# Kernel optimization log

Hardware: AMD Instinct MI355X
Metric: run time of the kernel (lower is better)

The kernel has to match this reference:

```python
import jax, jax.numpy as jnp
import numpy as np

B, N, H, KRATE = 128, 400, 128, 0.2
EPS = 1e-9


def setup_inputs() -> dict:
    key = jax.random.key(0)
    ks = jax.random.split(key, 16)
    # correlation-like input: symmetric, values in (-1,1), unit diagonal
    x = jax.random.normal(ks[0], (B, N, N), dtype=jnp.float32)
    x = jnp.tanh(0.3 * x)
    x = 0.5 * (x + x.transpose(0, 2, 1))
    eye = jnp.eye(N, dtype=jnp.float32)
    x = x * (1.0 - eye) + eye

    def lin(k, fan_in, shape):
        return jax.random.normal(k, shape, dtype=jnp.float32) / np.sqrt(fan_in).astype(np.float32)

    return {
        "x": x,
        "slength": jnp.full((B,), 100, dtype=jnp.int32),
        # AE denoiser (num_of_node=N, hidden=H)
        "enc1_w": lin(ks[1], N, (N, H)), "enc1_b": jnp.zeros((H,), jnp.float32),
        "enc2_w": lin(ks[2], N, (N, H)), "enc2_b": jnp.zeros((H,), jnp.float32),
        "dec2_w": lin(ks[3], H, (H, N)), "dec2_b": jnp.zeros((N,), jnp.float32),
        "dec1_w": lin(ks[4], H, (H, N)), "dec1_b": jnp.zeros((N,), jnp.float32),
        # GCN predictor
        "gcn1_w": lin(ks[5], N, (N, H)), "gcn1_b": jnp.zeros((H,), jnp.float32),
        "gcn2_w": lin(ks[6], H, (H, H)), "gcn2_b": jnp.zeros((H,), jnp.float32),
        # classification head Linear(128 -> 2)
        "fc_w": lin(ks[7], H, (H, 2)), "fc_b": jnp.zeros((2,), jnp.float32),
    }


def reference(x, slength, enc1_w, enc1_b, enc2_w, enc2_b, dec2_w, dec2_b,
              dec1_w, dec1_b, gcn1_w, gcn1_b, gcn2_w, gcn2_b, fc_w, fc_b):
    eye = jnp.eye(N, dtype=x.dtype)

    # fisher transform + normalize by [0,0] entry
    xf = 0.5 * jnp.log((1.0 + x + EPS) / (1.0 - x + EPS))
    xf = xf / xf[:, 0, 0][:, None, None]

    # --- DA / AE denoiser: deltax = AE(xf), symmetrized ---
    out1 = jax.nn.relu(jnp.einsum('bij,jh->bih', xf, enc1_w) + enc1_b).transpose(0, 2, 1)  # [B,H,N]
    out2 = jax.nn.relu(jnp.einsum('bhn,nk->bhk', out1, enc2_w) + enc2_b)                   # [B,H,H]
    out2 = jax.nn.relu(jnp.einsum('bhk,kn->bhn', out2, dec2_w) + dec2_b + out1)            # [B,H,N]
    out2 = out2.transpose(0, 2, 1)                                                         # [B,N,H]
    delta = jnp.einsum('bnh,hm->bnm', out2, dec1_w) + dec1_b                               # [B,N,N]
    delta = 0.5 * (delta + delta.transpose(0, 2, 1))
    x2 = xf + delta * (1.0 - eye)

    # --- predictor on detached x2 ---
    xp = jax.lax.stop_gradient(x2)

    # topk sparsification at rate 0.2 over flattened NxN per sample
    k = int(N * N * KRATE)
    flat = xp.reshape(B, N * N)
    _, idx = jax.lax.top_k(flat, k)
    mask = jnp.zeros((B, N * N), xp.dtype).at[jnp.arange(B)[:, None], idx].set(1.0)
    A = xp * mask.reshape(B, N, N)

    # GCN norm (PyG gcn_norm with add_remaining_self_loops, fill=1)
    diag = jnp.diagonal(A, axis1=1, axis2=2)
    A = A + eye[None] * jnp.where(diag == 0.0, 1.0, 0.0)[:, :, None]
    deg = A.sum(axis=1)                      # scatter of edge weight on col index
    dinv = deg ** -0.5
    dinv = jnp.where(jnp.isinf(dinv), 0.0, dinv)
    An = dinv[:, :, None] * A * dinv[:, None, :]  # An[b,i,j] = dinv[i]*A[i,j]*dinv[j]

    # GCNConv1 -> ReLU -> GCNConv2 (aggregate onto col/target index)
    h = jax.nn.relu(jnp.einsum('bij,bif->bjf', An, xp @ gcn1_w) + gcn1_b)  # [B,N,H]
    h = jnp.einsum('bij,bif->bjf', An, h @ gcn2_w) + gcn2_b                # [B,N,H]

    pooled = h.mean(axis=1)                  # mean over nodes -> [B,H]
    out = jax.nn.relu(pooled) @ fc_w + fc_b  # [B,2]
    return out
```

## Files before the change

### kernel.cpp

```cpp
#include <hip/hip_runtime.h>
#include <hip/hip_bf16.h>
#include <math.h>

#define BATCH 128
#define NNODE 400
#define HID   128
#define NN    (NNODE*NNODE)
#define KSEL  32000
#define EQCAP 1024
#define EPSF  1e-9f
#define TSPLIT 8
#define SEG   (NN / TSPLIT)
#define NT    7
#define KC400 14
#define FRAGS (KC400*4096)
#define PLA   57344

__device__ __forceinline__ unsigned tokey(float f) {
  unsigned u = __float_as_uint(f);
  return (u & 0x80000000u) ? ~u : (u | 0x80000000u);
}

__device__ __forceinline__ short f2bf(float f) {
  unsigned u = __float_as_uint(f);
  u += 0x7fffu + ((u >> 16) & 1u);
  return (short)(u >> 16);
}
__device__ __forceinline__ float bf2f(short s) {
  return __uint_as_float(((unsigned)(unsigned short)s) << 16);
}

__device__ __forceinline__ float xfhw(float xv, float cmul) {
  float la = __builtin_amdgcn_logf(1.0f + xv + EPSF);
  float lb = __builtin_amdgcn_logf(1.0f - xv + EPSF);
  return (la - lb) * cmul;
}

typedef __attribute__((ext_vector_type(8))) short s8v;
typedef __attribute__((ext_vector_type(4))) short s4v;
typedef __attribute__((ext_vector_type(4))) float f4v;

#define BK 16
#define LP 68

template<bool AT, bool BIAS, bool RES, bool RELU, bool TS>
__global__ void __launch_bounds__(256) gemm64(
    const float* __restrict__ A, long sA, int lda,
    const float* __restrict__ B, long sB, int ldb,
    const float* __restrict__ bias,
    const float* __restrict__ Res, long sRes,
    float* __restrict__ C, long sC, int ldc,
    int M, int Nc, int K)
{
  __shared__ float As[BK][LP];
  __shared__ float Bs[BK][LP];
  const int bz = blockIdx.z;
  A += (size_t)bz * sA;
  B += (size_t)bz * sB;
  C += (size_t)bz * sC;
  const float* Rp = RES ? (Res + (size_t)bz * sRes) : nullptr;

  const int n0 = blockIdx.x * 64;
  const int m0 = blockIdx.y * 64;
  const int tid = threadIdx.x;
  const int tx = tid & 15, ty = tid >> 4;
  const bool edgeM = (m0 + 64 > M);
  const bool edgeN = (n0 + 64 > Nc);

  float acc[4][4];
#pragma unroll
  for (int i = 0; i < 4; ++i)
#pragma unroll
    for (int j = 0; j < 4; ++j) acc[i][j] = 0.f;

  for (int k0 = 0; k0 < K; k0 += BK) {
    if (!AT) {
      const int m = tid & 63, g = tid >> 6;
      if (!edgeM) {
        const float4 v = *(const float4*)(A + (size_t)(m0 + m) * lda + k0 + 4 * g);
        As[4 * g + 0][m] = v.x; As[4 * g + 1][m] = v.y;
        As[4 * g + 2][m] = v.z; As[4 * g + 3][m] = v.w;
      } else {
        const int gm = m0 + m;
        const bool ok = gm < M;
#pragma unroll
        for (int j = 0; j < 4; ++j)
          As[4 * g + j][m] = ok ? A[(size_t)gm * lda + k0 + 4 * g + j] : 0.f;
      }
    } else {
      const int k = tid >> 4, mg = tid & 15;
      if (!edgeM) {
        const float4 v = *(const float4*)(A + (size_t)(k0 + k) * lda + m0 + 4 * mg);
        *(float4*)&As[k][4 * mg] = v;
      } else {
#pragma unroll
        for (int j = 0; j < 4; ++j) {
          const int gm = m0 + 4 * mg + j;
          As[k][4 * mg + j] = (gm < M) ? A[(size_t)(k0 + k) * lda + gm] : 0.f;
        }
      }
    }
    {
      const int k = tid >> 4, ng = tid & 15;
      if (!edgeN) {
        const float4 v = *(const float4*)(B + (size_t)(k0 + k) * ldb + n0 + 4 * ng);
        *(float4*)&Bs[k][4 * ng] = v;
      } else {
#pragma unroll
        for (int j = 0; j < 4; ++j) {
          const int gn = n0 + 4 * ng + j;
          Bs[k][4 * ng + j] = (gn < Nc) ? B[(size_t)(k0 + k) * ldb + gn] : 0.f;
        }
      }
    }
    __syncthreads();
#pragma unroll
    for (int kk = 0; kk < BK; ++kk) {
      const float4 a = *(const float4*)&As[kk][ty << 2];
      const float4 b = *(const float4*)&Bs[kk][tx << 2];
      const float av[4] = {a.x, a.y, a.z, a.w};
      const float bv[4] = {b.x, b.y, b.z, b.w};
#pragma unroll
      for (int i = 0; i < 4; ++i)
#pragma unroll
        for (int j = 0; j < 4; ++j) acc[i][j] += av[i] * bv[j];
    }
    __syncthreads();
  }

#pragma unroll
  for (int i = 0; i < 4; ++i) {
    const int m = m0 + (ty << 2) + i;
    if (m >= M) continue;
#pragma unroll
    for (int j = 0; j < 4; ++j) {
      const int n = n0 + (tx << 2) + j;
      if (n >= Nc) continue;
      float v = acc[i][j];
      if (BIAS) v += bias[n];
      const size_t loc = TS ? ((size_t)n * ldc + m) : ((size_t)m * ldc + n);
      if (RES) v += Rp[loc];
      if (RELU) v = fmaxf(v, 0.f);
      C[loc] = v;
    }
  }
}

__global__ void bsplit5(
    const float* __restrict__ gcn1_w, const float* __restrict__ gcn2_w,
    const float* __restrict__ enc1_w, const float* __restrict__ enc2_w,
    const float* __restrict__ dec1_w,
    short* __restrict__ w1frag, short* __restrict__ w2frag,
    short* __restrict__ e1frag, short* __restrict__ e2frag,
    short* __restrict__ dfrag) {
  const float* W; short* out; int K, Kpad, N, Npad;
  switch (blockIdx.y) {
    case 0: W = gcn1_w; out = w1frag; K = NNODE; Kpad = 448; N = HID;   Npad = 128; break;
    case 1: W = gcn2_w; out = w2frag; K = HID;   Kpad = 128; N = HID;   Npad = 128; break;
    case 2: W = enc1_w; out = e1frag; K = NNODE; Kpad = 448; N = HID;   Npad = 128; break;
    case 3: W = enc2_w; out = e2frag; K = NNODE; Kpad = 448; N = HID;   Npad = 128; break;
    default: W = dec1_w; out = dfrag; K = HID;   Kpad = 128; N = NNODE; Npad = 448; break;
  }
  int t = blockIdx.x * 256 + threadIdx.x;
  if (t >= Kpad * Npad) return;
  int k = t / Npad, n = t - k * Npad;
  float v = (k < K && n < N) ? W[(size_t)k * N + n] : 0.f;
  short hi = f2bf(v);
  short lo = f2bf(v - bf2f(hi));
  int ntiles = Npad >> 4;
  size_t idx = (((size_t)(k >> 5) * ntiles + (n >> 4)) * 64
                + (((k >> 3) & 3) * 16 + (n & 15))) * 8 + (k & 7);
  size_t PL = (size_t)(Kpad >> 5) * ntiles * 512;
  out[idx] = hi;
  out[PL + idx] = lo;
}

template<bool AT, bool FRAG, bool BIAS, bool RELU, bool SCL, bool TS, bool XF>
__global__ void __launch_bounds__(256) mfgemm(
    const float* __restrict__ A, long sA, int lda,
    const short* __restrict__ Bf, long sB, int kc,
    const float* __restrict__ bias,
    const float* __restrict__ scl,
    float* __restrict__ Cf, long sCf, int ldc,
    short* __restrict__ Cfrag, long sCfrag, int okc,
    const float* __restrict__ denomp, float* __restrict__ xfout,
    int M, int K)
{
  __shared__ float As[64][68];
  const int bz = blockIdx.y;
  A += (size_t)bz * sA;
  Bf += (size_t)bz * sB;
  if (SCL) scl += (size_t)bz * NNODE;
  if (!FRAG) Cf += (size_t)bz * sCf;
  else       Cfrag += (size_t)bz * sCfrag;
  if (XF) xfout += (size_t)bz * sA;
  const float cmul = XF ? (0.34657359027997264f / denomp[bz]) : 0.f;

  const int tid = threadIdx.x;
  const int lane = tid & 63, wave = tid >> 6;
  const int wqm = wave >> 1, wqn = wave & 1;
  const int quad = lane >> 4, l15 = lane & 15;
  const int m0 = blockIdx.x * 64;

  f4v acc[2][4];
#pragma unroll
  for (int i = 0; i < 2; ++i)
#pragma unroll
    for (int j = 0; j < 4; ++j) acc[i][j] = (f4v){0.f, 0.f, 0.f, 0.f};

  const int nstage = (K + 63) >> 6;
  for (int st = 0; st < nstage; ++st) {
    const int k0 = st << 6;
    if (st) __syncthreads();
    if (!AT) {
      const int mrow = tid >> 4;
      const int k4 = (tid & 15) << 2;
#pragma unroll
      for (int u = 0; u < 4; ++u) {
        const int m = mrow + (u << 4);
        const int gm = m0 + m, gk = k0 + k4;
        float4 v = {0.f, 0.f, 0.f, 0.f};
        if (gm < M) {
          if (gk + 4 <= K) {
            float4 xv = *(const float4*)(A + (size_t)gm * lda + gk);
            if (XF) {
              v.x = xfhw(xv.x, cmul);
              v.y = xfhw(xv.y, cmul);
              v.z = xfhw(xv.z, cmul);
              v.w = xfhw(xv.w, cmul);
              *(float4*)(xfout + (size_t)gm * lda + gk) = v;
            } else v = xv;
          } else {
            float* pv = (float*)&v;
#pragma unroll
            for (int j = 0; j < 4; ++j)
              if (gk + j < K) {
                float xv = A[(size_t)gm * lda + gk + j];
                if (XF) {
                  pv[j] = xfhw(xv, cmul);
                  xfout[(size_t)gm * lda + gk + j] = pv[j];
                } else pv[j] = xv;
              }
          }
        }
        *(float4*)&As[m][k4] = v;
      }
    } else {
      const int kk = tid >> 4;
      const int m4 = (tid & 15) << 2;
#pragma unroll
      for (int u = 0; u < 4; ++u) {
        const int gk = k0 + kk + (u << 4);
        float4 v = {0.f, 0.f, 0.f, 0.f};
        if (gk < K) {
          if (m0 + m4 + 4 <= M) v = *(const float4*)(A + (size_t)gk * lda + m0 + m4);
          else {
            float* pv = (float*)&v;
#pragma unroll
            for (int j = 0; j < 4; ++j)
              if (m0 + m4 + j < M) pv[j] = A[(size_t)gk * lda + m0 + m4 + j];
          }
        }
        As[m4 + 0][kk + (u << 4)] = v.x;
        As[m4 + 1][kk + (u << 4)] = v.y;
        As[m4 + 2][kk + (u << 4)] = v.z;
        As[m4 + 3][kk + (u << 4)] = v.w;
      }
    }
    __syncthreads();

#pragma unroll
    for (int c2 = 0; c2 < 2; ++c2) {
      const int c = (st << 1) + c2;
      s8v bhi[4], blo[4];
#pragma unroll
      for (int nt = 0; nt < 4; ++nt) {
        const int ntg = (wqn << 2) + nt;
        const size_t off = (((size_t)c * 8 + ntg) * 64 + lane) * 8;
        bhi[nt] = *(const s8v*)(Bf + off);
        blo[nt] = *(const s8v*)(Bf + (size_t)kc * 4096 + off);
      }
#pragma unroll
      for (int mt = 0; mt < 2; ++mt) {
        const int row = (wqm << 5) + (mt << 4) + l15;
        const int kof = (c2 << 5) + (quad << 3);
        const f4v a0 = *(const f4v*)&As[row][kof];
        const f4v a1 = *(const f4v*)&As[row][kof + 4];
        s8v ah, al;
#pragma unroll
        for (int j = 0; j < 4; ++j) {
          short h0 = f2bf(a0[j]); ah[j] = h0; al[j] = f2bf(a0[j] - bf2f(h0));
          short h1 = f2bf(a1[j]); ah[j + 4] = h1; al[j + 4] = f2bf(a1[j] - bf2f(h1));
        }
#pragma unroll
        for (int nt = 0; nt < 4; ++nt) {
          acc[mt][nt] = __builtin_amdgcn_mfma_f32_16x16x32_bf16(ah, bhi[nt], acc[mt][nt], 0, 0, 0);
          acc[mt][nt] = __builtin_amdgcn_mfma_f32_16x16x32_bf16(ah, blo[nt], acc[mt][nt], 0, 0, 0);
          acc[mt][nt] = __builtin_amdgcn_mfma_f32_16x16x32_bf16(al, bhi[nt], acc[mt][nt], 0, 0, 0);
        }
      }
    }
  }

  if (TS) {
    for (int nh = 0; nh < 2; ++nh) {
      __syncthreads();
      if (wqn == nh) {
#pragma unroll
        for (int mt = 0; mt < 2; ++mt)
#pragma unroll
          for (int nt = 0; nt < 4; ++nt) {
            const int tn = (nt << 4) + l15;
            const int n  = (wqn << 6) + tn;
            const int mc = (wqm << 5) + (mt << 4) + (quad << 2);
            const f4v a = acc[mt][nt];
#pragma unroll
            for (int reg = 0; reg < 4; ++reg) {
              float v = a[reg];
              if (SCL) v *= scl[m0 + mc + reg];
              if (BIAS) v += bias[n];
              if (RELU) v = fmaxf(v, 0.f);
              As[tn][mc + reg] = v;
            }
          }
      }
      __syncthreads();
      const int row = tid >> 2, cq = tid & 3;
#pragma unroll
      for (int u = 0; u < 4; ++u) {
        const int col = (cq + (u << 2)) << 2;
        if (m0 + col + 4 <= M) {
          const float4 v = *(const float4*)&As[row][col];
          *(float4*)(Cf + (size_t)((nh << 6) + row) * ldc + m0 + col) = v;
        }
      }
    }
    return;
  }

#pragma unroll
  for (int mt = 0; mt < 2; ++mt) {
    const int mb = m0 + (wqm << 5) + (mt << 4) + (quad << 2);
#pragma unroll
    for (int nt = 0; nt < 4; ++nt) {
      const int n = (wqn << 6) + (nt << 4) + l15;
      const f4v a = acc[mt][nt];
      if (!FRAG) {
#pragma unroll
        for (int reg = 0; reg < 4; ++reg) {
          const int m = mb + reg;
          if (m < M) {
            float v = a[reg];
            if (SCL) v *= scl[m];
            if (BIAS) v += bias[n];
            if (RELU) v = fmaxf(v, 0.f);
            Cf[(size_t)m * ldc + n] = v;
          }
        }
      } else {
        s4v h4, l4;
#pragma unroll
        for (int reg = 0; reg < 4; ++reg) {
          const int m = mb + reg;
          float v = (m < M) ? (SCL ? a[reg] * scl[m] : a[reg]) : 0.f;
          short hh = f2bf(v);
          h4[reg] = hh; l4[reg] = f2bf(v - bf2f(hh));
        }
        const int chunkT = mb >> 5, quadT = (mb >> 3) & 3, jT0 = mb & 7;
        const size_t off = (((size_t)chunkT * 8 + (wqn << 2) + nt) * 64
                            + quadT * 16 + l15) * 8 + jT0;
        *(s4v*)(Cfrag + off) = h4;
        *(s4v*)(Cfrag + (size_t)okc * 4096 + off) = l4;
      }
    }
  }
}

__global__ void __launch_bounds__(256) g4mf(
    const float* __restrict__ o1,
    const short* __restrict__ wfrag,
    const float* __restrict__ bias,
    float* __restrict__ xf,
    unsigned* __restrict__ ghist)
{
  __shared__ float D2[64][68];
  __shared__ unsigned hist[2048];
  const int b = blockIdx.y;
  int p = blockIdx.x, bi = 0;
  while (p >= NT - bi) { p -= NT - bi; ++bi; }
  const int bj = bi + p;
  const int I0 = bi * 64, J0 = bj * 64;
  const bool diag = (bi == bj);

  o1 += (size_t)b * HID * NNODE;
  xf += (size_t)b * NN;
  unsigned* gh = ghist + (size_t)b * 4096;

  const int tid = threadIdx.x;
  const int lane = tid & 63, wave = tid >> 6;
  const int wq = wave & 1;
  const bool d1 = wave < 2;
  const int Bt = (d1 ? bj : bi) * 4;
  const int quad = lane >> 4, l15 = lane & 15;
  const int M0 = d1 ? I0 : J0;

  for (int i = tid; i < 2048; i += 256) hist[i] = 0u;

  f4v acc[2][4];
#pragma unroll
  for (int i = 0; i < 2; ++i)
#pragma unroll
    for (int j = 0; j < 4; ++j) acc[i][j] = (f4v){0.f, 0.f, 0.f, 0.f};

  const int gm0 = M0 + (wq << 5) + l15;

  for (int c = 0; c < 4; ++c) {
    const int k0 = c << 5;
    s8v bhi[4], blo[4];
#pragma unroll
    for (int nt = 0; nt < 4; ++nt) {
      const int ntg = Bt + nt;
      const size_t off = (((size_t)c * 28 + ntg) * 64 + lane) * 8;
      bhi[nt] = *(const s8v*)(wfrag + off);
      blo[nt] = *(const s8v*)(wfrag + PLA + off);
    }
#pragma unroll
    for (int mt = 0; mt < 2; ++mt) {
      const int gm = gm0 + (mt << 4);
      float av[8];
      if (gm < NNODE) {
        const float* cp = o1 + (size_t)(k0 + (quad << 3)) * NNODE + gm;
#pragma unroll
        for (int j = 0; j < 8; ++j) av[j] = cp[(size_t)j * NNODE];
      } else {
#pragma unroll
        for (int j = 0; j < 8; ++j) av[j] = 0.f;
      }
      s8v ah, al;
#pragma unroll
      for (int j = 0; j < 8; ++j) {
        short h = f2bf(av[j]); ah[j] = h; al[j] = f2bf(av[j] - bf2f(h));
      }
#pragma unroll
      for (int nt = 0; nt < 4; ++nt) {
        acc[mt][nt] = __builtin_amdgcn_mfma_f32_16x16x32_bf16(ah, bhi[nt], acc[mt][nt], 0, 0, 0);
        acc[mt][nt] = __builtin_amdgcn_mfma_f32_16x16x32_bf16(ah, blo[nt], acc[mt][nt], 0, 0, 0);
        acc[mt][nt] = __builtin_amdgcn_mfma_f32_16x16x32_bf16(al, bhi[nt], acc[mt][nt], 0, 0, 0);
      }
    }
  }

  if (!d1) {
#pragma unroll
    for (int mt = 0; mt < 2; ++mt) {
      const int mb = (wq << 5) + (mt << 4) + (quad << 2);
#pragma unroll
      for (int nt = 0; nt < 4; ++nt) {
        const int nn = (nt << 4) + l15;
        const f4v a = acc[mt][nt];
#pragma unroll
        for (int reg = 0; reg < 4; ++reg) D2[mb + reg][nn] = a[reg];
      }
    }
  }
  __syncthreads();

  if (d1) {
    const unsigned w = diag ? 1u : 2u;
#pragma unroll
    for (int mt = 0; mt < 2; ++mt) {
      const int a0 = (wq << 5) + (mt << 4) + (quad << 2);
#pragma unroll
      for (int nt = 0; nt < 4; ++nt) {
        const int nn = (nt << 4) + l15;
        const int gj = J0 + nn;
        const f4v d1v = acc[mt][nt];
        const f4v d2t = *(const f4v*)&D2[nn][a0];
        f4v vv;
#pragma unroll
        for (int reg = 0; reg < 4; ++reg) {
          const int gi = I0 + a0 + reg;
          float v = 0.f;
          if (gi < NNODE && gj < NNODE) {
            v = xf[(size_t)gi * NNODE + gj];
            if (gi != gj)
              v += 0.5f * (d1v[reg] + d2t[reg] + bias[gj] + bias[gi]);
            const unsigned bin = tokey(v) >> 20;
            atomicAdd(&hist[bin >> 1], w << ((bin & 1) << 4));
          }
          vv[reg] = v;
        }
#pragma unroll
        for (int reg = 0; reg < 4; ++reg) {
          const int gi = I0 + a0 + reg;
          if (gi < NNODE && gj < NNODE) xf[(size_t)gi * NNODE + gj] = vv[reg];
        }
        if (!diag && gj < NNODE && (I0 + a0 + 4 <= NNODE)) {
          *(float4*)(xf + (size_t)gj * NNODE + I0 + a0) = *(float4*)&vv;
        }
      }
    }
  }
  __syncthreads();
  for (int i = tid; i < 2048; i += 256) {
    const unsigned v = hist[i];
    const unsigned lo = v & 0xFFFFu, hi = v >> 16;
    if (lo) atomicAdd(&gh[2 * i], lo);
    if (hi) atomicAdd(&gh[2 * i + 1], hi);
  }
}

__global__ void tzd(const float* __restrict__ x, unsigned* __restrict__ ghist,
                    unsigned* __restrict__ sprefix, int* __restrict__ sk,
                    int* __restrict__ eqcnt, float* __restrict__ deg,
                    float* __restrict__ denom) {
  int t = blockIdx.x * 256 + threadIdx.x;
  if (t < BATCH * 4096) ghist[t] = 0u;
  if (t < BATCH) {
    sprefix[t] = 0u; sk[t] = KSEL; eqcnt[t] = 0;
    float v = x[(size_t)t * NN];
    denom[t] = 0.5f * logf((1.0f + v + EPSF) / (1.0f - v + EPSF));
  }
  if (t < BATCH * NNODE) deg[t] = 0.f;
}

__global__ void __launch_bounds__(256) thistA(const float* __restrict__ x2,
                                              const unsigned* __restrict__ sprefix,
                                              unsigned* __restrict__ ghist) {
  __shared__ unsigned h[4096];
  const int b  = blockIdx.y;
  const int sb = blockIdx.x;
  const int tid = threadIdx.x;
  for (int i = tid; i < 4096; i += 256) h[i] = 0u;
  __syncthreads();

  const unsigned prefix = sprefix[b];
  const float4* p4 = (const float4*)(x2 + (size_t)b * NN);
  const int i0 = sb * (SEG / 4), i1 = i0 + (SEG / 4);
  for (int i = i0 + tid; i < i1; i += 256) {
    float4 v = p4[i];
    unsigned k0 = tokey(v.x), k1 = tokey(v.y), k2 = tokey(v.z), k3 = tokey(v.w);
    if ((k0 & 0xFFF00000u) == prefix) atomicAdd(&h[(k0 >> 8) & 4095u], 1u);
    if ((k1 & 0xFFF00000u) == prefix) atomicAdd(&h[(k1 >> 8) & 4095u], 1u);
    if ((k2 & 0xFFF00000u) == prefix) atomicAdd(&h[(k2 >> 8) & 4095u], 1u);
    if ((k3 & 0xFFF00000u) == prefix) atomicAdd(&h[(k3 >> 8) & 4095u], 1u);
  }
  __syncthreads();
  for (int i = tid; i < 4096; i += 256) {
    unsigned s = h[i];
    if (s) atomicAdd(&ghist[(size_t)b * 4096 + i], s);
  }
}

__global__ void __launch_bounds__(256) thistB(const float* __restrict__ x2,
                                              const unsigned* __restrict__ sprefix,
                                              unsigned* __restrict__ ghist) {
  __shared__ unsigned h[8][256];
  const int b  = blockIdx.y;
  const int sb = blockIdx.x;
  const int tid = threadIdx.x;
  for (int i = tid; i < 8 * 256; i += 256) ((unsigned*)h)[i] = 0u;
  __syncthreads();

  const unsigned prefix = sprefix[b];
  const int rep = tid & 7;
  const float4* p4 = (const float4*)(x2 + (size_t)b * NN);
  const int i0 = sb * (SEG / 4), i1 = i0 + (SEG / 4);
  for (int i = i0 + tid; i < i1; i += 256) {
    float4 v = p4[i];
    unsigned k0 = tokey(v.x), k1 = tokey(v.y), k2 = tokey(v.z), k3 = tokey(v.w);
    if ((k0 & 0xFFFFFF00u) == prefix) atomicAdd(&h[rep][k0 & 255u], 1u);
    if ((k1 & 0xFFFFFF00u) == prefix) atomicAdd(&h[rep][k1 & 255u], 1u);
    if ((k2 & 0xFFFFFF00u) == prefix) atomicAdd(&h[rep][k2 & 255u], 1u);
    if ((k3 & 0xFFFFFF00u) == prefix) atomicAdd(&h[rep][k3 & 255u], 1u);
  }
  __syncthreads();
  if (tid < 256) {
    unsigned s = h[0][tid] + h[1][tid] + h[2][tid] + h[3][tid]
               + h[4][tid] + h[5][tid] + h[6][tid] + h[7][tid];
    if (s) atomicAdd(&ghist[(size_t)b * 4096 + tid], s);
  }
}

template<int SH>
__global__ void __launch_bounds__(256) tpick12(unsigned* __restrict__ ghist,
                                               unsigned* __restrict__ sprefix,
                                               int* __restrict__ sk) {
  const int b = blockIdx.x;
  __shared__ unsigned h[4096];
  __shared__ unsigned csum[256];
  unsigned* gh = ghist + (size_t)b * 4096;
  unsigned local = 0;
#pragma unroll
  for (int u = 0; u < 16; ++u) {
    unsigned v = gh[threadIdx.x * 16 + u];
    h[threadIdx.x * 16 + u] = v;
    local += v;
  }
  csum[threadIdx.x] = local;
  __syncthreads();
  if (threadIdx.x == 0) {
    int k = sk[b];
    int bin = 0;
    for (int ch = 255; ch >= 0; --ch) {
      int S = (int)csum[ch];
      if (S >= k) {
        for (int bb = ch * 16 + 15; bb >= ch * 16; --bb) {
          int c = (int)h[bb];
          if (c >= k) { bin = bb; break; }
          k -= c;
        }
        break;
      }
      k -= S;
    }
    sprefix[b] = sprefix[b] | ((unsigned)bin << SH);
    sk[b] = k;
  }
#pragma unroll
  for (int u = 0; u < 16; ++u) gh[threadIdx.x * 16 + u] = 0u;
}

__global__ void __launch_bounds__(256) tpick8f(const unsigned* __restrict__ ghist,
                                               const unsigned* __restrict__ sprefix,
                                               const int* __restrict__ sk,
                                               unsigned* __restrict__ tau,
                                               int* __restrict__ rrem) {
  const int b = blockIdx.x;
  __shared__ unsigned h[256];
  h[threadIdx.x] = ghist[(size_t)b * 4096 + threadIdx.x];
  __syncthreads();
  if (threadIdx.x == 0) {
    int k = sk[b];
    unsigned byte = 0u;
    for (int bin = 255; bin >= 0; --bin) {
      int c = (int)h[bin];
      if (c >= k) { byte = (unsigned)bin; break; }
      k -= c;
    }
    tau[b] = sprefix[b] | byte;
    rrem[b] = k;
  }
}

__global__ void __launch_bounds__(256) build_kc(
    const float* __restrict__ x2, const unsigned* __restrict__ tau,
    float* __restrict__ A, float* __restrict__ deg,
    int* __restrict__ eqcnt, int* __restrict__ eqidx) {
  __shared__ float cs[NNODE];
  const int b = blockIdx.y, rg = blockIdx.x;
  const int tid = threadIdx.x;
  for (int i = tid; i < NNODE; i += 256) cs[i] = 0.f;
  __syncthreads();
  const unsigned tk = tau[b];
  const size_t base = (size_t)b * NN + (size_t)rg * 6400;
  for (int u = 0; u < 25; ++u) {
    const int t = u * 256 + tid;
    const float v = x2[base + t];
    const unsigned key = tokey(v);
    const float a = (key > tk) ? v : 0.f;
    A[base + t] = a;
    if (key == tk) {
      int p = atomicAdd(&eqcnt[b], 1);
      if (p < EQCAP) eqidx[b * EQCAP + p] = rg * 6400 + t;
    }
    if (a != 0.f) atomicAdd(&cs[t % NNODE], a);
  }
  __syncthreads();
  for (int j = tid; j < NNODE; j += 256)
    if (cs[j] != 0.f) atomicAdd(&deg[b * NNODE + j], cs[j]);
}

__global__ void __launch_bounds__(256) eqdinv(
    float* __restrict__ A, const float* __restrict__ x2,
    float* __restrict__ deg, float* __restrict__ dinv,
    const int* __restrict__ eqcnt, const int* __restrict__ eqidx,
    const int* __restrict__ rrem) {
  const int b = blockIdx.x;
  int cnt = eqcnt[b]; if (cnt > EQCAP) cnt = EQCAP;
  const int r = rrem[b];
  for (int t = threadIdx.x; t < cnt; t += 256) {
    int idx = eqidx[b * EQCAP + t];
    int rank = 0;
    for (int u = 0; u < cnt; ++u) rank += (eqidx[b * EQCAP + u] < idx) ? 1 : 0;
    if (rank < r) {
      float v = x2[(size_t)b * NN + idx];
      A[(size_t)b * NN + idx] = v;
      atomicAdd(&deg[b * NNODE + idx % NNODE], v);
    }
  }
  __syncthreads();
  for (int j = threadIdx.x; j < NNODE; j += 256) {
    float d = deg[b * NNODE + j];
    size_t o = (size_t)b * NN + (size_t)j * NNODE + j;
    if (A[o] == 0.f) { A[o] = 1.0f; d += 1.0f; }
    dinv[b * NNODE + j] = (d == 0.f) ? 0.f : 1.0f / sqrtf(d);
  }
}

__global__ void head_k(const float* __restrict__ h2, const float* __restrict__ fc_w,
                       const float* __restrict__ fc_b, float* __restrict__ out) {
  int b = blockIdx.x;
  int f = threadIdx.x;
  float s = 0.f;
  const float* p = h2 + (size_t)b * NNODE * HID + f;
  for (int j = 0; j < NNODE; ++j) s += p[(size_t)j * HID];
  float pv = fmaxf(s / (float)NNODE, 0.f);
  __shared__ float r0[128], r1[128];
  r0[f] = pv * fc_w[f * 2 + 0];
  r1[f] = pv * fc_w[f * 2 + 1];
  __syncthreads();
  for (int sft = 64; sft > 0; sft >>= 1) {
    if (f < sft) { r0[f] += r0[f + sft]; r1[f] += r1[f + sft]; }
    __syncthreads();
  }
  if (f == 0) {
    out[b * 2 + 0] = r0[0] + fc_b[0];
    out[b * 2 + 1] = r1[0] + fc_b[1];
  }
}

extern "C" void kernel_launch(void* const* d_in, const int* in_sizes, int n_in,
                              void* d_out, int out_size, void* d_ws, size_t ws_size,
                              hipStream_t stream) {
  const float* x      = (const float*)d_in[0];
  const float* enc1_w = (const float*)d_in[2];
  const float* enc1_b = (const float*)d_in[3];
  const float* enc2_w = (const float*)d_in[4];
  const float* enc2_b = (const float*)d_in[5];
  const float* dec2_w = (const float*)d_in[6];
  const float* dec2_b = (const float*)d_in[7];
  const float* dec1_w = (const float*)d_in[8];
  const float* dec1_b = (const float*)d_in[9];
  const float* gcn1_w = (const float*)d_in[10];
  const float* gcn1_b = (const float*)d_in[11];
  const float* gcn2_w = (const float*)d_in[12];
  const float* gcn2_b = (const float*)d_in[13];
  const float* fc_w   = (const float*)d_in[14];
  const float* fc_b   = (const float*)d_in[15];
  float* out = (float*)d_out;
  (void)in_sizes; (void)n_in; (void)out_size; (void)ws_size;

  float* ws = (float*)d_ws;
  size_t off = 0;
  auto take = [&](size_t n) { float* p = ws + off; off += (n + 63) & ~(size_t)63; return p; };
  float* xf   = take((size_t)BATCH * NN);
  float* dl   = take((size_t)BATCH * NN);
  float* o1   = take((size_t)BATCH * HID * NNODE);
  float* o2   = take((size_t)BATCH * HID * HID);
  float* hbuf = take((size_t)BATCH * NNODE * HID);
  float* denom = take(BATCH);
  float* dinv  = take((size_t)BATCH * NNODE);
  float* deg   = take((size_t)BATCH * NNODE);
  unsigned* tau = (unsigned*)take(BATCH);
  int* rrem  = (int*)take(BATCH);
  int* eqcnt = (int*)take(BATCH);
  int* eqidx = (int*)take((size_t)BATCH * EQCAP);
  unsigned* ghist   = (unsigned*)take((size_t)BATCH * 4096);
  unsigned* sprefix = (unsigned*)take(BATCH);
  int*      sk      = (int*)take(BATCH);
  short* w1frag = (short*)take((size_t)FRAGS + 64);
  short* w2frag = (short*)take((size_t)4 * 4096 + 64);
  short* e1frag = (short*)take((size_t)FRAGS + 64);
  short* e2frag = (short*)take((size_t)FRAGS + 64);
  short* dfrag  = (short*)take((size_t)PLA + 64);
  short* xwfrag = (short*)o1;
  const long sXW = 2L * FRAGS;

  tzd<<<2048, 256, 0, stream>>>(x, ghist, sprefix, sk, eqcnt, deg, denom);
  bsplit5<<<dim3(224, 5), 256, 0, stream>>>(gcn1_w, gcn2_w, enc1_w, enc2_w, dec1_w,
                                            w1frag, w2frag, e1frag, e2frag, dfrag);

  mfgemm<false, false, true, true, false, true, true><<<dim3(7, BATCH), 256, 0, stream>>>(
      x, NN, NNODE, e1frag, 0, KC400, enc1_b, nullptr,
      o1, (long)HID * NNODE, NNODE, nullptr, 0, 0, denom, xf, NNODE, NNODE);
  mfgemm<false, false, true, true, false, false, false><<<dim3(2, BATCH), 256, 0, stream>>>(
      o1, (long)HID * NNODE, NNODE, e2frag, 0, KC400, enc2_b, nullptr,
      o2, (long)HID * HID, HID, nullptr, 0, 0, nullptr, nullptr, HID, NNODE);
  gemm64<false, true, true, true, false><<<dim3(7, 2, BATCH), 256, 0, stream>>>(
      o2, (long)HID * HID, HID, dec2_w, 0, NNODE, dec2_b,
      o1, (long)HID * NNODE, o1, (long)HID * NNODE, NNODE, HID, NNODE, HID);

  g4mf<<<dim3(NT * (NT + 1) / 2, BATCH), 256, 0, stream>>>(o1, dfrag, dec1_b, xf, ghist);

  tpick12<20><<<BATCH, 256, 0, stream>>>(ghist, sprefix, sk);
  thistA<<<dim3(TSPLIT, BATCH), 256, 0, stream>>>(xf, sprefix, ghist);
  tpick12<8><<<BATCH, 256, 0, stream>>>(ghist, sprefix, sk);
  thistB<<<dim3(TSPLIT, BATCH), 256, 0, stream>>>(xf, sprefix, ghist);
  tpick8f<<<BATCH, 256, 0, stream>>>(ghist, sprefix, sk, tau, rrem);

  build_kc<<<dim3(25, BATCH), 256, 0, stream>>>(xf, tau, dl, deg, eqcnt, eqidx);
  eqdinv<<<BATCH, 256, 0, stream>>>(dl, xf, deg, dinv, eqcnt, eqidx, rrem);

  mfgemm<false, true, false, false, true, false, false><<<dim3(7, BATCH), 256, 0, stream>>>(
      xf, NN, NNODE, w1frag, 0, KC400, nullptr, dinv,
      nullptr, 0, 128, xwfrag, sXW, KC400, nullptr, nullptr, NNODE, NNODE);
  mfgemm<true, false, true, true, true, false, false><<<dim3(7, BATCH), 256, 0, stream>>>(
      dl, NN, NNODE, xwfrag, sXW, KC400, gcn1_b, dinv,
      hbuf, (long)NNODE * HID, HID, nullptr, 0, 0, nullptr, nullptr, NNODE, NNODE);
  mfgemm<false, true, false, false, true, false, false><<<dim3(7, BATCH), 256, 0, stream>>>(
      hbuf, (long)NNODE * HID, HID, w2frag, 0, 4, nullptr, dinv,
      nullptr, 0, 128, xwfrag, sXW, KC400, nullptr, nullptr, NNODE, HID);
  mfgemm<true, false, true, false, true, false, false><<<dim3(7, BATCH), 256, 0, stream>>>(
      dl, NN, NNODE, xwfrag, sXW, KC400, gcn2_b, dinv,
      hbuf, (long)NNODE * HID, HID, nullptr, 0, 0, nullptr, nullptr, NNODE, NNODE);

  head_k<<<BATCH, HID, 0, stream>>>(hbuf, fc_w, fc_b, out);
}
```

Measured before the change: 651.6 us.

## Compact radix-select candidates in pass A to skip a full rescan in pass B

The second histogram pass now writes the keys that match the 12-bit prefix into a per-sample candidate buffer (reusing the dl workspace), using wave ballot and an atomic counter. The final 8-bit histogram and threshold pick are fused into one kernel that reads only those candidates instead of rescanning the full NxN matrix. This removes one full read of x2 per sample and one kernel launch. In exchange it adds global atomics and scattered writes in thistA, and the fused pick kernel runs one block per sample.

```diff
diff --git a/kernel.cpp b/kernel.cpp
--- a/kernel.cpp
+++ b/kernel.cpp
@@ -513,11 +513,11 @@
 __global__ void tzd(const float* __restrict__ x, unsigned* __restrict__ ghist,
                     unsigned* __restrict__ sprefix, int* __restrict__ sk,
                     int* __restrict__ eqcnt, float* __restrict__ deg,
-                    float* __restrict__ denom) {
+                    float* __restrict__ denom, unsigned* __restrict__ ccnt) {
   int t = blockIdx.x * 256 + threadIdx.x;
   if (t < BATCH * 4096) ghist[t] = 0u;
   if (t < BATCH) {
-    sprefix[t] = 0u; sk[t] = KSEL; eqcnt[t] = 0;
+    sprefix[t] = 0u; sk[t] = KSEL; eqcnt[t] = 0; ccnt[t] = 0u;
     float v = x[(size_t)t * NN];
     denom[t] = 0.5f * logf((1.0f + v + EPSF) / (1.0f - v + EPSF));
   }
@@ -526,59 +526,42 @@
 
 __global__ void __launch_bounds__(256) thistA(const float* __restrict__ x2,
                                               const unsigned* __restrict__ sprefix,
-                                              unsigned* __restrict__ ghist) {
+                                              unsigned* __restrict__ ghist,
+                                              unsigned* __restrict__ cand,
+                                              unsigned* __restrict__ ccnt) {
   __shared__ unsigned h[4096];
   const int b  = blockIdx.y;
   const int sb = blockIdx.x;
   const int tid = threadIdx.x;
+  const int lane = tid & 63;
   for (int i = tid; i < 4096; i += 256) h[i] = 0u;
   __syncthreads();
 
   const unsigned prefix = sprefix[b];
+  unsigned* cb = cand + (size_t)b * NN;
   const float4* p4 = (const float4*)(x2 + (size_t)b * NN);
   const int i0 = sb * (SEG / 4), i1 = i0 + (SEG / 4);
   for (int i = i0 + tid; i < i1; i += 256) {
     float4 v = p4[i];
-    unsigned k0 = tokey(v.x), k1 = tokey(v.y), k2 = tokey(v.z), k3 = tokey(v.w);
-    if ((k0 & 0xFFF00000u) == prefix) atomicAdd(&h[(k0 >> 8) & 4095u], 1u);
-    if ((k1 & 0xFFF00000u) == prefix) atomicAdd(&h[(k1 >> 8) & 4095u], 1u);
-    if ((k2 & 0xFFF00000u) == prefix) atomicAdd(&h[(k2 >> 8) & 4095u], 1u);
-    if ((k3 & 0xFFF00000u) == prefix) atomicAdd(&h[(k3 >> 8) & 4095u], 1u);
+    unsigned kk[4] = {tokey(v.x), tokey(v.y), tokey(v.z), tokey(v.w)};
+#pragma unroll
+    for (int q = 0; q < 4; ++q) {
+      const unsigned key = kk[q];
+      const bool m = (key & 0xFFF00000u) == prefix;
+      if (m) atomicAdd(&h[(key >> 8) & 4095u], 1u);
+      const unsigned long long bal = __ballot(m);
+      if (bal) {
+        unsigned base = 0;
+        if (lane == 0) base = atomicAdd(&ccnt[b], (unsigned)__popcll(bal));
+        base = __shfl(base, 0);
+        if (m) cb[base + __popcll(bal & ((1ull << lane) - 1ull))] = key;
+      }
+    }
   }
   __syncthreads();
   for (int i = tid; i < 4096; i += 256) {
     unsigned s = h[i];
     if (s) atomicAdd(&ghist[(size_t)b * 4096 + i], s);
-  }
-}
-
-__global__ void __launch_bounds__(256) thistB(const float* __restrict__ x2,
-                                              const unsigned* __restrict__ sprefix,
-                                              unsigned* __restrict__ ghist) {
-  __shared__ unsigned h[8][256];
-  const int b  = blockIdx.y;
-  const int sb = blockIdx.x;
-  const int tid = threadIdx.x;
-  for (int i = tid; i < 8 * 256; i += 256) ((unsigned*)h)[i] = 0u;
-  __syncthreads();
-
-  const unsigned prefix = sprefix[b];
-  const int rep = tid & 7;
-  const float4* p4 = (const float4*)(x2 + (size_t)b * NN);
-  const int i0 = sb * (SEG / 4), i1 = i0 + (SEG / 4);
-  for (int i = i0 + tid; i < i1; i += 256) {
-    float4 v = p4[i];
-    unsigned k0 = tokey(v.x), k1 = tokey(v.y), k2 = tokey(v.z), k3 = tokey(v.w);
-    if ((k0 & 0xFFFFFF00u) == prefix) atomicAdd(&h[rep][k0 & 255u], 1u);
-    if ((k1 & 0xFFFFFF00u) == prefix) atomicAdd(&h[rep][k1 & 255u], 1u);
-    if ((k2 & 0xFFFFFF00u) == prefix) atomicAdd(&h[rep][k2 & 255u], 1u);
-    if ((k3 & 0xFFFFFF00u) == prefix) atomicAdd(&h[rep][k3 & 255u], 1u);
-  }
-  __syncthreads();
-  if (tid < 256) {
-    unsigned s = h[0][tid] + h[1][tid] + h[2][tid] + h[3][tid]
-               + h[4][tid] + h[5][tid] + h[6][tid] + h[7][tid];
-    if (s) atomicAdd(&ghist[(size_t)b * 4096 + tid], s);
   }
 }
 
@@ -621,24 +604,41 @@
   for (int u = 0; u < 16; ++u) gh[threadIdx.x * 16 + u] = 0u;
 }
 
-__global__ void __launch_bounds__(256) tpick8f(const unsigned* __restrict__ ghist,
-                                               const unsigned* __restrict__ sprefix,
-                                               const int* __restrict__ sk,
-                                               unsigned* __restrict__ tau,
-                                               int* __restrict__ rrem) {
+__global__ void __launch_bounds__(256) thistC(const unsigned* __restrict__ cand,
+                                              const unsigned* __restrict__ ccnt,
+                                              const unsigned* __restrict__ sprefix,
+                                              const int* __restrict__ sk,
+                                              unsigned* __restrict__ tau,
+                                              int* __restrict__ rrem) {
+  __shared__ unsigned h[8][256];
   const int b = blockIdx.x;
-  __shared__ unsigned h[256];
-  h[threadIdx.x] = ghist[(size_t)b * 4096 + threadIdx.x];
-  __syncthreads();
-  if (threadIdx.x == 0) {
+  const int tid = threadIdx.x;
+  for (int i = tid; i < 8 * 256; i += 256) ((unsigned*)h)[i] = 0u;
+  __syncthreads();
+  const unsigned prefix = sprefix[b];
+  const unsigned n = ccnt[b];
+  const unsigned* cp = cand + (size_t)b * NN;
+  const int rep = tid & 7;
+  for (unsigned i = tid; i < n; i += 256) {
+    const unsigned key = cp[i];
+    if ((key & 0xFFFFFF00u) == prefix) atomicAdd(&h[rep][key & 255u], 1u);
+  }
+  __syncthreads();
+  if (tid < 256) {
+    const unsigned s = h[0][tid] + h[1][tid] + h[2][tid] + h[3][tid]
+                     + h[4][tid] + h[5][tid] + h[6][tid] + h[7][tid];
+    h[0][tid] = s;
+  }
+  __syncthreads();
+  if (tid == 0) {
     int k = sk[b];
     unsigned byte = 0u;
     for (int bin = 255; bin >= 0; --bin) {
-      int c = (int)h[bin];
+      int c = (int)h[0][bin];
       if (c >= k) { byte = (unsigned)bin; break; }
       k -= c;
     }
-    tau[b] = sprefix[b] | byte;
+    tau[b] = prefix | byte;
     rrem[b] = k;
   }
 }
@@ -759,15 +759,17 @@
   unsigned* ghist   = (unsigned*)take((size_t)BATCH * 4096);
   unsigned* sprefix = (unsigned*)take(BATCH);
   int*      sk      = (int*)take(BATCH);
+  unsigned* ccnt    = (unsigned*)take(BATCH);
   short* w1frag = (short*)take((size_t)FRAGS + 64);
   short* w2frag = (short*)take((size_t)4 * 4096 + 64);
   short* e1frag = (short*)take((size_t)FRAGS + 64);
   short* e2frag = (short*)take((size_t)FRAGS + 64);
   short* dfrag  = (short*)take((size_t)PLA + 64);
   short* xwfrag = (short*)o1;
+  unsigned* cand = (unsigned*)dl;
   const long sXW = 2L * FRAGS;
 
-  tzd<<<2048, 256, 0, stream>>>(x, ghist, sprefix, sk, eqcnt, deg, denom);
+  tzd<<<2048, 256, 0, stream>>>(x, ghist, sprefix, sk, eqcnt, deg, denom, ccnt);
   bsplit5<<<dim3(224, 5), 256, 0, stream>>>(gcn1_w, gcn2_w, enc1_w, enc2_w, dec1_w,
                                             w1frag, w2frag, e1frag, e2frag, dfrag);
 
@@ -784,10 +786,9 @@
   g4mf<<<dim3(NT * (NT + 1) / 2, BATCH), 256, 0, stream>>>(o1, dfrag, dec1_b, xf, ghist);
 
   tpick12<20><<<BATCH, 256, 0, stream>>>(ghist, sprefix, sk);
-  thistA<<<dim3(TSPLIT, BATCH), 256, 0, stream>>>(xf, sprefix, ghist);
+  thistA<<<dim3(TSPLIT, BATCH), 256, 0, stream>>>(xf, sprefix, ghist, cand, ccnt);
   tpick12<8><<<BATCH, 256, 0, stream>>>(ghist, sprefix, sk);
-  thistB<<<dim3(TSPLIT, BATCH), 256, 0, stream>>>(xf, sprefix, ghist);
-  tpick8f<<<BATCH, 256, 0, stream>>>(ghist, sprefix, sk, tau, rrem);
+  thistC<<<BATCH, 256, 0, stream>>>(cand, ccnt, sprefix, sk, tau, rrem);
 
   build_kc<<<dim3(25, BATCH), 256, 0, stream>>>(xf, tau, dl, deg, eqcnt, eqidx);
   eqdinv<<<BATCH, 256, 0, stream>>>(dl, xf, deg, dinv, eqcnt, eqidx, rrem);
```

Result: slower. 1.242 ms (+90.6%).
